# Kernel tuning notes

Measured on AMD Instinct MI355X. Metric: run time of the kernel, lower is better.

## Reference

```python
import jax, jax.numpy as jnp
import numpy as np

N = 50000       # n_user == n_item (required by torch.cat(dim=1) in the source)
E = 800000      # edges per relation (avg degree 16)
NEG_SLOPE = 0.2 # DGL GATConv default


def gat_conv(x, W, a_l, a_r, b, src, dst, n_dst):
    """DGL GATConv: x [Ns,F], W [F,H*O], a_l/a_r/b [H,O], src/dst [E] -> [n_dst,H,O]."""
    H, O = a_l.shape
    h = (x @ W).reshape(-1, H, O)                     # projected features [Ns,H,O]
    el = jnp.sum(h * a_l, axis=-1)                    # [Ns,H]
    er = jnp.sum(h * a_r, axis=-1)                    # [Ns,H] (src feats reused as dst feats, as in source)
    e = jax.nn.leaky_relu(el[src] + er[dst], NEG_SLOPE)   # per-edge scores [E,H]
    # numerically-stable segment softmax over incoming edges of each dst node
    m = jax.ops.segment_max(e, dst, num_segments=n_dst)  # [n_dst,H]
    ee = jnp.exp(e - m[dst])
    denom = jax.ops.segment_sum(ee, dst, num_segments=n_dst)
    alpha = ee / denom[dst]                           # [E,H]
    out = jax.ops.segment_sum(alpha[:, :, None] * h[src], dst, num_segments=n_dst)
    return out + b                                    # [n_dst,H,O]


def setup_inputs() -> dict:
    key = jax.random.key(0)
    ks = jax.random.split(key, 12)
    inp = {
        "x": jax.random.normal(ks[0], (N, 32), jnp.float32),
        "W1": jax.random.normal(ks[1], (32, 128), jnp.float32) * 0.1,   # [in, H*hidden]
        "aL1": jax.random.normal(ks[2], (2, 64), jnp.float32) * 0.1,
        "aR1": jax.random.normal(ks[3], (2, 64), jnp.float32) * 0.1,
        "b1": jnp.zeros((2, 64), jnp.float32),
        "W2": jax.random.normal(ks[4], (256, 2), jnp.float32) * 0.1,    # [4*hidden, H*out]
        "aL2": jax.random.normal(ks[5], (2, 1), jnp.float32) * 0.1,
        "aR2": jax.random.normal(ks[6], (2, 1), jnp.float32) * 0.1,
        "b2": jnp.zeros((2, 1), jnp.float32),
        "src_follows": jax.random.randint(ks[7], (E,), 0, N, jnp.int32),
        "dst_follows": jax.random.randint(ks[8], (E,), 0, N, jnp.int32),
        "src_likes": jax.random.randint(ks[9], (E,), 0, N, jnp.int32),
        "dst_likes": jax.random.randint(ks[10], (E,), 0, N, jnp.int32),
    }
    return inp


def reference(x, W1, aL1, aR1, b1, W2, aL2, aR2, b2,
              src_follows, dst_follows, src_likes, dst_likes):
    # layer 1: shared conv1 applied to both relations
    h1_f = gat_conv(x, W1, aL1, aR1, b1, src_follows, dst_follows, N)  # [N,2,64]
    h1_l = gat_conv(x, W1, aL1, aR1, b1, src_likes, dst_likes, N)      # [N,2,64]
    h1 = jnp.concatenate([h1_f, h1_l], axis=1).reshape(N, -1)          # [N,256]
    # layer 2: shared conv2 applied to both relations
    h2_f = gat_conv(h1, W2, aL2, aR2, b2, src_follows, dst_follows, N)  # [N,2,1]
    h2_l = gat_conv(h1, W2, aL2, aR2, b2, src_likes, dst_likes, N)      # [N,2,1]
    return jnp.concatenate([h2_f, h2_l], axis=1)                        # [N,4,1]
```

## Files before the change

### kernel.cpp

```cpp
#include <hip/hip_runtime.h>

#define LREL(x) ((x) > 0.0f ? (x) : 0.2f * (x))
#define TILE 391
#define NT 128
#define NP (2 * NT)
#define PSTRIDE (TILE + 1)
#define CAP 7680
#define PB 512
#define CAP2 32

__device__ __forceinline__ unsigned bf16rne(float f) {
    unsigned u = __float_as_uint(f);
    return (u + 0x7FFFu + ((u >> 16) & 1u)) >> 16;
}

__global__ __launch_bounds__(256) void k_projbuild(
        const float* __restrict__ x, const float* __restrict__ W1,
        const float* __restrict__ aL1, const float* __restrict__ aR1,
        const float* __restrict__ W2,
        float* __restrict__ recA, float* __restrict__ recB, float* __restrict__ er1,
        const int* __restrict__ srcF, const int* __restrict__ dstF,
        const int* __restrict__ srcL, const int* __restrict__ dstL,
        int* __restrict__ part, int* __restrict__ cnt, int N, int E, int projB) {
    __shared__ float ps[384];
    __shared__ int cur[NP];
    int tid = threadIdx.x;
    if ((int)blockIdx.x < projB) {
        for (int i = tid; i < 384; i += 256) {
            int k = i / 12, q = i % 12;
            float acc = 0.f;
            if (q < 2) {
                int h = q;
#pragma unroll
                for (int o = 0; o < 64; ++o) acc = fmaf(W1[k * 128 + h * 64 + o], aL1[h * 64 + o], acc);
            } else if (q < 4) {
                int h = q - 2;
#pragma unroll
                for (int o = 0; o < 64; ++o) acc = fmaf(W1[k * 128 + h * 64 + o], aR1[h * 64 + o], acc);
            } else {
                int r = q - 4;
                int rel = r >> 2, h = (r >> 1) & 1, kk = r & 1;
#pragma unroll
                for (int o = 0; o < 64; ++o)
                    acc = fmaf(W1[k * 128 + h * 64 + o], W2[(rel * 128 + h * 64 + o) * 2 + kk], acc);
            }
            ps[i] = acc;
        }
        __syncthreads();
        int n = blockIdx.x * 256 + tid;
        if (n >= N) return;
        float xr[32];
#pragma unroll
        for (int u = 0; u < 8; ++u) {
            float4 v = *(const float4*)(x + (long)n * 32 + u * 4);
            xr[u * 4 + 0] = v.x; xr[u * 4 + 1] = v.y;
            xr[u * 4 + 2] = v.z; xr[u * 4 + 3] = v.w;
        }
        float o[12];
#pragma unroll
        for (int q = 0; q < 12; ++q) o[q] = 0.f;
#pragma unroll
        for (int k = 0; k < 32; ++k) {
            float xv = xr[k];
#pragma unroll
            for (int q = 0; q < 12; ++q) o[q] = fmaf(xv, ps[k * 12 + q], o[q]);
        }
        *(float2*)(er1 + 2 * n) = make_float2(o[2], o[3]);
        float4 ra, rb;
        ra.x = o[0]; ra.y = o[1];
        ra.z = __uint_as_float(bf16rne(o[4]) | (bf16rne(o[5]) << 16));
        ra.w = __uint_as_float(bf16rne(o[6]) | (bf16rne(o[7]) << 16));
        rb.x = o[0]; rb.y = o[1];
        rb.z = __uint_as_float(bf16rne(o[8]) | (bf16rne(o[9]) << 16));
        rb.w = __uint_as_float(bf16rne(o[10]) | (bf16rne(o[11]) << 16));
        *(float4*)(recA + (long)n * 4) = ra;
        *(float4*)(recB + (long)n * 4) = rb;
    } else {
        int b = blockIdx.x - projB;
        cur[tid] = 0;
        __syncthreads();
        int chunk = (((E + PB - 1) / PB) + 1) & ~1;
        int lo = b * chunk, hi = lo + chunk;
        if (hi > E) hi = E; if (lo > E) lo = E;
        int m = (hi - lo) >> 1;
        const int2* dF2 = (const int2*)(dstF + lo);
        const int2* sF2 = (const int2*)(srcF + lo);
        const int2* dL2 = (const int2*)(dstL + lo);
        const int2* sL2 = (const int2*)(srcL + lo);
        for (int i = tid; i < m; i += 256) {
            int2 d2 = dF2[i], s2 = sF2[i];
            int tA = d2.x / TILE, tB = d2.y / TILE;
            int pxA = (s2.x << 9) | (d2.x - tA * TILE);
            int pxB = (s2.y << 9) | (d2.y - tB * TILE);
            int slA = atomicAdd(&cur[tA], 1);
            int slB = atomicAdd(&cur[tB], 1);
            int2 e2 = dL2[i], t2 = sL2[i];
            int tC = e2.x / TILE, tD = e2.y / TILE;
            int pxC = (t2.x << 9) | (e2.x - tC * TILE);
            int pxD = (t2.y << 9) | (e2.y - tD * TILE);
            int slC = atomicAdd(&cur[NT + tC], 1);
            int slD = atomicAdd(&cur[NT + tD], 1);
            if (slA < CAP2) part[((long)b * NP + tA) * CAP2 + slA] = pxA;
            if (slB < CAP2) part[((long)b * NP + tB) * CAP2 + slB] = pxB;
            if (slC < CAP2) part[((long)b * NP + NT + tC) * CAP2 + slC] = pxC;
            if (slD < CAP2) part[((long)b * NP + NT + tD) * CAP2 + slD] = pxD;
        }
        if (tid == 0 && ((hi - lo) & 1)) {
            int e = hi - 1;
            int d = dstF[e];
            int t = d / TILE;
            int sl = atomicAdd(&cur[t], 1);
            if (sl < CAP2) part[((long)b * NP + t) * CAP2 + sl] = (srcF[e] << 9) | (d - t * TILE);
            d = dstL[e];
            t = d / TILE;
            sl = atomicAdd(&cur[NT + t], 1);
            if (sl < CAP2) part[((long)b * NP + NT + t) * CAP2 + sl] = (srcL[e] << 9) | (d - t * TILE);
        }
        __syncthreads();
        int c = cur[tid];
        cnt[tid * PB + b] = c < CAP2 ? c : CAP2;
    }
}

__global__ __launch_bounds__(1024) void k_sort(const int* __restrict__ part,
                                               const int* __restrict__ cnt,
                                               int* __restrict__ part2,
                                               int* __restrict__ offd) {
    __shared__ int sub[PB + 1];
    __shared__ int ls[1024];
    __shared__ int hist[TILE];
    __shared__ int cur[TILE];
    __shared__ int pxS[CAP];
    int p = blockIdx.x, tid = threadIdx.x;
    int c = (tid < PB) ? cnt[p * PB + tid] : 0;
    ls[tid] = (tid < PB) ? c : 0;
    __syncthreads();
    for (int o = 1; o < PB; o <<= 1) {
        int t = (tid >= o && tid < PB) ? ls[tid - o] : 0;
        __syncthreads();
        if (tid < PB) ls[tid] += t;
        __syncthreads();
    }
    if (tid < PB) sub[tid] = ls[tid] - c;
    if (tid == 0) sub[PB] = ls[PB - 1];
    __syncthreads();
    int len = sub[PB]; if (len > CAP) len = CAP;
    for (int j = tid; j < len; j += 1024) {
        int loB = 0, hiB = PB;
        while (hiB - loB > 1) {
            int mid = (loB + hiB) >> 1;
            if (sub[mid] <= j) loB = mid; else hiB = mid;
        }
        pxS[j] = part[((long)loB * NP + p) * CAP2 + (j - sub[loB])];
    }
    for (int i = tid; i < TILE; i += 1024) hist[i] = 0;
    __syncthreads();
    for (int j = tid; j < len; j += 1024) atomicAdd(&hist[pxS[j] & 511], 1);
    __syncthreads();
    int v = (tid < TILE) ? hist[tid] : 0;
    ls[tid] = v;
    __syncthreads();
    for (int o = 1; o < 1024; o <<= 1) {
        int t = (tid >= o) ? ls[tid - o] : 0;
        __syncthreads();
        ls[tid] += t;
        __syncthreads();
    }
    int base = p * CAP;
    if (tid < TILE) {
        int s = base + ls[tid] - v;
        offd[p * PSTRIDE + tid] = s;
        cur[tid] = s;
    }
    if (tid == 0) offd[p * PSTRIDE + TILE] = base + len;
    __syncthreads();
    for (int j = tid; j < len; j += 1024) {
        int px = pxS[j];
        int slot = atomicAdd(&cur[px & 511], 1);
        part2[slot] = px >> 9;
    }
}

__global__ __launch_bounds__(256) void k_agg1(
        const int* __restrict__ part2, const int* __restrict__ offd,
        const float* __restrict__ recA, const float* __restrict__ recB,
        const float* __restrict__ er1, const float* __restrict__ b1,
        const float* __restrict__ W2, float* __restrict__ h2, int N) {
    __shared__ float4 sh[32];
    __shared__ float bkS[2];
    if (threadIdx.x < 2) {
        int k = threadIdx.x;
        float acc = 0.f;
#pragma unroll
        for (int c = 0; c < 256; ++c) acc = fmaf(b1[c & 127], W2[c * 2 + k], acc);
        bkS[k] = acc;
    }
    int gt = (blockIdx.x * 256 + threadIdx.x) >> 3;
    int r = threadIdx.x & 7;
    int d = gt >> 1, rel = gt & 1;
    bool valid = d < N;
    float4 res = make_float4(0.f, 0.f, 0.f, 0.f);
    if (valid) {
        int tile = d / TILE, dl = d - tile * TILE;
        int idx = (rel * NT + tile) * PSTRIDE + dl;
        int j0 = offd[idx], j1 = offd[idx + 1];
        float2 er = *(const float2*)(er1 + 2 * d);
        const float* R = rel ? recB : recA;
        float n00 = 0.f, n01 = 0.f, n10 = 0.f, n11 = 0.f, w0s = 0.f, w1s = 0.f;
        for (int j = j0 + r; j < j1; j += 8) {
            int sn = part2[j];
            float4 v = *(const float4*)(R + (long)sn * 4);
            unsigned p01 = __float_as_uint(v.z), p23 = __float_as_uint(v.w);
            float g0 = __uint_as_float(p01 << 16), g1 = __uint_as_float(p01 & 0xFFFF0000u);
            float g2 = __uint_as_float(p23 << 16), g3 = __uint_as_float(p23 & 0xFFFF0000u);
            float w0 = __expf(LREL(v.x + er.x));
            float w1 = __expf(LREL(v.y + er.y));
            n00 = fmaf(w0, g0, n00);
            n01 = fmaf(w0, g1, n01);
            n10 = fmaf(w1, g2, n10);
            n11 = fmaf(w1, g3, n11);
            w0s += w0;
            w1s += w1;
        }
#pragma unroll
        for (int o = 1; o < 8; o <<= 1) {
            n00 += __shfl_xor(n00, o);
            n01 += __shfl_xor(n01, o);
            n10 += __shfl_xor(n10, o);
            n11 += __shfl_xor(n11, o);
            w0s += __shfl_xor(w0s, o);
            w1s += __shfl_xor(w1s, o);
        }
        if (j1 > j0) {
            res.x = n00 / w0s; res.y = n01 / w0s;
            res.z = n10 / w1s; res.w = n11 / w1s;
        }
    }
    if (r == 0) sh[threadIdx.x >> 3] = res;
    __syncthreads();
    if (valid && rel == 0 && r == 0) {
        float4 q = sh[(threadIdx.x >> 3) + 1];
        *(float2*)(h2 + 2 * d) =
            make_float2(bkS[0] + res.x + res.z + q.x + q.z,
                        bkS[1] + res.y + res.w + q.y + q.w);
    }
}

__global__ __launch_bounds__(256) void k_agg2(
        const int* __restrict__ part2, const int* __restrict__ offd,
        const float* __restrict__ h2, const float* __restrict__ aL2,
        const float* __restrict__ aR2, const float* __restrict__ b2,
        float* __restrict__ out, int N) {
    int gt = (blockIdx.x * 256 + threadIdx.x) >> 3;
    int r = threadIdx.x & 7;
    int d = gt >> 1, rel = gt & 1;
    if (d >= N) return;
    int tile = d / TILE, dl = d - tile * TILE;
    int idx = (rel * NT + tile) * PSTRIDE + dl;
    int j0 = offd[idx], j1 = offd[idx + 1];
    float aL0 = aL2[0], aL1_ = aL2[1];
    float2 hd = *(const float2*)(h2 + 2 * d);
    float e0 = hd.x * aR2[0], e1 = hd.y * aR2[1];
    float n0 = 0.f, n1 = 0.f, s0 = 0.f, s1 = 0.f;
    for (int j = j0 + r; j < j1; j += 8) {
        int sn = part2[j];
        float2 hs = *(const float2*)(h2 + 2 * sn);
        float w0 = __expf(LREL(hs.x * aL0 + e0));
        float w1 = __expf(LREL(hs.y * aL1_ + e1));
        n0 = fmaf(w0, hs.x, n0);
        n1 = fmaf(w1, hs.y, n1);
        s0 += w0;
        s1 += w1;
    }
#pragma unroll
    for (int o = 1; o < 8; o <<= 1) {
        n0 += __shfl_xor(n0, o);
        n1 += __shfl_xor(n1, o);
        s0 += __shfl_xor(s0, o);
        s1 += __shfl_xor(s1, o);
    }
    if (r == 0) {
        int deg = j1 - j0;
        *(float2*)(out + (long)d * 4 + rel * 2) =
            make_float2((deg ? n0 / s0 : 0.f) + b2[0], (deg ? n1 / s1 : 0.f) + b2[1]);
    }
}

extern "C" void kernel_launch(void* const* d_in, const int* in_sizes, int n_in,
                              void* d_out, int out_size, void* d_ws, size_t ws_size,
                              hipStream_t stream) {
    const float* x   = (const float*)d_in[0];
    const float* W1  = (const float*)d_in[1];
    const float* aL1 = (const float*)d_in[2];
    const float* aR1 = (const float*)d_in[3];
    const float* b1  = (const float*)d_in[4];
    const float* W2  = (const float*)d_in[5];
    const float* aL2 = (const float*)d_in[6];
    const float* aR2 = (const float*)d_in[7];
    const float* b2  = (const float*)d_in[8];
    const int* srcF  = (const int*)d_in[9];
    const int* dstF  = (const int*)d_in[10];
    const int* srcL  = (const int*)d_in[11];
    const int* dstL  = (const int*)d_in[12];
    float* out = (float*)d_out;

    const int N = in_sizes[0] / 32;
    const int E = in_sizes[9];
    const int projB = (N + 255) / 256;

    float* ws   = (float*)d_ws;
    float* recA = ws;
    float* recB = recA + (long)4 * N;
    float* er1  = recB + (long)4 * N;
    float* h2   = er1 + (long)2 * N;
    int* part   = (int*)(h2 + (long)2 * N);
    int* part2  = part + (long)PB * NP * CAP2;
    int* cnt    = part2 + (long)NP * CAP;
    int* offd   = cnt + NP * PB;

    k_projbuild<<<projB + PB, 256, 0, stream>>>(x, W1, aL1, aR1, W2, recA, recB, er1,
                                                srcF, dstF, srcL, dstL, part, cnt, N, E, projB);
    k_sort<<<NP, 1024, 0, stream>>>(part, cnt, part2, offd);

    int ab = (2 * N * 8 + 255) / 256;
    k_agg1<<<ab, 256, 0, stream>>>(part2, offd, recA, recB, er1, b1, W2, h2, N);
    k_agg2<<<ab, 256, 0, stream>>>(part2, offd, h2, aL2, aR2, b2, out, N);
}
```

Baseline: 72.86 us.

## Stage edge bins in shared memory and write compacted partitions per block

The partition pass now scatters packed edges into shared-memory bins, then prefix-sums bin counts and writes each block's bins contiguously to a compact slot region with a per-bin offset table. The sort kernel copies each source block's run directly using that offset instead of a per-element binary search over block prefix sums. The aim is to shrink the global footprint of the intermediate partitions and remove the search cost. In exchange, the copy loops are serial per thread with uncoalesced strides, and the build kernel uses more shared memory, which may lower occupancy.

```diff
diff --git a/kernel.cpp b/kernel.cpp
--- a/kernel.cpp
+++ b/kernel.cpp
@@ -8,6 +8,7 @@
 #define CAP 7680
 #define PB 512
 #define CAP2 32
+#define SLOTB 3200
 
 __device__ __forceinline__ unsigned bf16rne(float f) {
     unsigned u = __float_as_uint(f);
@@ -21,9 +22,12 @@
         float* __restrict__ recA, float* __restrict__ recB, float* __restrict__ er1,
         const int* __restrict__ srcF, const int* __restrict__ dstF,
         const int* __restrict__ srcL, const int* __restrict__ dstL,
-        int* __restrict__ part, int* __restrict__ cnt, int N, int E, int projB) {
+        int* __restrict__ part, int* __restrict__ cnt, int* __restrict__ loc,
+        int N, int E, int projB) {
     __shared__ float ps[384];
+    __shared__ int bins[NP * CAP2];
     __shared__ int cur[NP];
+    __shared__ int lsb[NP];
     int tid = threadIdx.x;
     if ((int)blockIdx.x < projB) {
         for (int i = tid; i < 384; i += 256) {
@@ -100,30 +104,43 @@
             int pxD = (t2.y << 9) | (e2.y - tD * TILE);
             int slC = atomicAdd(&cur[NT + tC], 1);
             int slD = atomicAdd(&cur[NT + tD], 1);
-            if (slA < CAP2) part[((long)b * NP + tA) * CAP2 + slA] = pxA;
-            if (slB < CAP2) part[((long)b * NP + tB) * CAP2 + slB] = pxB;
-            if (slC < CAP2) part[((long)b * NP + NT + tC) * CAP2 + slC] = pxC;
-            if (slD < CAP2) part[((long)b * NP + NT + tD) * CAP2 + slD] = pxD;
+            if (slA < CAP2) bins[tA * CAP2 + slA] = pxA;
+            if (slB < CAP2) bins[tB * CAP2 + slB] = pxB;
+            if (slC < CAP2) bins[(NT + tC) * CAP2 + slC] = pxC;
+            if (slD < CAP2) bins[(NT + tD) * CAP2 + slD] = pxD;
         }
         if (tid == 0 && ((hi - lo) & 1)) {
             int e = hi - 1;
             int d = dstF[e];
             int t = d / TILE;
             int sl = atomicAdd(&cur[t], 1);
-            if (sl < CAP2) part[((long)b * NP + t) * CAP2 + sl] = (srcF[e] << 9) | (d - t * TILE);
+            if (sl < CAP2) bins[t * CAP2 + sl] = (srcF[e] << 9) | (d - t * TILE);
             d = dstL[e];
             t = d / TILE;
             sl = atomicAdd(&cur[NT + t], 1);
-            if (sl < CAP2) part[((long)b * NP + NT + t) * CAP2 + sl] = (srcL[e] << 9) | (d - t * TILE);
-        }
-        __syncthreads();
-        int c = cur[tid];
-        cnt[tid * PB + b] = c < CAP2 ? c : CAP2;
+            if (sl < CAP2) bins[(NT + t) * CAP2 + sl] = (srcL[e] << 9) | (d - t * TILE);
+        }
+        __syncthreads();
+        int c = cur[tid]; if (c > CAP2) c = CAP2;
+        lsb[tid] = c;
+        __syncthreads();
+        for (int o = 1; o < NP; o <<= 1) {
+            int t = (tid >= o) ? lsb[tid - o] : 0;
+            __syncthreads();
+            lsb[tid] += t;
+            __syncthreads();
+        }
+        int off = lsb[tid] - c;
+        cnt[tid * PB + b] = c;
+        loc[tid * PB + b] = off;
+        long dstb = (long)b * SLOTB + off;
+        for (int i = 0; i < c; ++i) part[dstb + i] = bins[tid * CAP2 + i];
     }
 }
 
 __global__ __launch_bounds__(1024) void k_sort(const int* __restrict__ part,
                                                const int* __restrict__ cnt,
+                                               const int* __restrict__ loc,
                                                int* __restrict__ part2,
                                                int* __restrict__ offd) {
     __shared__ int sub[PB + 1];
@@ -145,13 +162,10 @@
     if (tid == 0) sub[PB] = ls[PB - 1];
     __syncthreads();
     int len = sub[PB]; if (len > CAP) len = CAP;
-    for (int j = tid; j < len; j += 1024) {
-        int loB = 0, hiB = PB;
-        while (hiB - loB > 1) {
-            int mid = (loB + hiB) >> 1;
-            if (sub[mid] <= j) loB = mid; else hiB = mid;
-        }
-        pxS[j] = part[((long)loB * NP + p) * CAP2 + (j - sub[loB])];
+    if (tid < PB) {
+        long srcb = (long)tid * SLOTB + loc[p * PB + tid];
+        int d0 = sub[tid];
+        for (int i = 0; i < c; ++i) pxS[d0 + i] = part[srcb + i];
     }
     for (int i = tid; i < TILE; i += 1024) hist[i] = 0;
     __syncthreads();
@@ -314,13 +328,15 @@
     float* er1  = recB + (long)4 * N;
     float* h2   = er1 + (long)2 * N;
     int* part   = (int*)(h2 + (long)2 * N);
-    int* part2  = part + (long)PB * NP * CAP2;
+    int* part2  = part + (long)PB * SLOTB;
     int* cnt    = part2 + (long)NP * CAP;
-    int* offd   = cnt + NP * PB;
+    int* loc    = cnt + NP * PB;
+    int* offd   = loc + NP * PB;
 
     k_projbuild<<<projB + PB, 256, 0, stream>>>(x, W1, aL1, aR1, W2, recA, recB, er1,
-                                                srcF, dstF, srcL, dstL, part, cnt, N, E, projB);
-    k_sort<<<NP, 1024, 0, stream>>>(part, cnt, part2, offd);
+                                                srcF, dstF, srcL, dstL, part, cnt, loc,
+                                                N, E, projB);
+    k_sort<<<NP, 1024, 0, stream>>>(part, cnt, loc, part2, offd);
 
     int ab = (2 * N * 8 + 255) / 256;
     k_agg1<<<ab, 256, 0, stream>>>(part2, offd, recA, recB, er1, b1, W2, h2, N);
```

After: 71.16 us. 2.3% less time.
